# Kernel tuning notes

Hardware: AMD Instinct MI355X
Metric: run time of the kernel (lower is better)

Reference implementation:

```python
import jax, jax.numpy as jnp
import numpy as np

D_MODEL = 1024
D_INNER = 2048
D_STATE = 16
D_CONV = 4
DT_RANK = 64
BATCH = 2
SEQ = 1024


def _silu(v):
    return v * jax.nn.sigmoid(v)


def setup_inputs() -> dict:
    key = jax.random.key(0)
    ks = jax.random.split(key, 8)
    s = 0.02
    return {
        "x": jax.random.normal(ks[0], (BATCH, SEQ, D_MODEL), jnp.float32),
        "norm_w": jnp.ones((D_MODEL,), jnp.float32),
        "in_proj_w": (jax.random.normal(ks[1], (2 * D_INNER, D_MODEL), jnp.float32) * s),
        "conv_w": (jax.random.normal(ks[2], (D_INNER, 1, D_CONV), jnp.float32) * s),
        "conv_b": jnp.zeros((D_INNER,), jnp.float32),
        "x_proj_w": (jax.random.normal(ks[3], (DT_RANK + 2 * D_STATE, D_INNER), jnp.float32) * s),
        "dt_proj_w": (jax.random.normal(ks[4], (D_INNER, DT_RANK), jnp.float32) * s),
        "dt_proj_b": jnp.zeros((D_INNER,), jnp.float32),
        "A_log": jnp.log(jnp.broadcast_to(jnp.arange(1, D_STATE + 1, dtype=jnp.float32), (D_INNER, D_STATE))),
        "D": jnp.ones((D_INNER,), jnp.float32),
        "out_proj_w": (jax.random.normal(ks[5], (D_MODEL, D_INNER), jnp.float32) * s),
    }


def reference(x, norm_w, in_proj_w, conv_w, conv_b, x_proj_w, dt_proj_w, dt_proj_b, A_log, D, out_proj_w):
    b, l, d = x.shape
    x_copy = x
    # MambaRMSNorm
    h = x * jax.lax.rsqrt(jnp.mean(x * x, axis=-1, keepdims=True) + 1e-5) * norm_w
    # in_proj -> split into x-path and residual gate
    x_and_res = h @ in_proj_w.T                       # [b, l, 2*d_inner]
    xs, res = jnp.split(x_and_res, 2, axis=-1)
    # causal depthwise conv1d (torch pads d_conv-1 both sides then slices [:l])
    xc = jnp.transpose(xs, (0, 2, 1))                 # [b, d_inner, l]
    xc = jax.lax.conv_general_dilated(
        xc, conv_w, window_strides=(1,), padding=[(D_CONV - 1, 0)],
        feature_group_count=D_INNER, dimension_numbers=("NCH", "OIH", "NCH"))
    xc = xc + conv_b[None, :, None]
    u = _silu(jnp.transpose(xc, (0, 2, 1)))           # [b, l, d_inner]
    # SSM parameters
    A = -jnp.exp(A_log)                               # [d_inner, n]
    x_dbl = u @ x_proj_w.T                            # [b, l, dt_rank + 2n]
    delta, Bm, Cm = jnp.split(x_dbl, [DT_RANK, DT_RANK + D_STATE], axis=-1)
    delta = jax.nn.softplus(delta @ dt_proj_w.T + dt_proj_b)   # [b, l, d_inner]
    deltaA = jnp.exp(jnp.einsum("bld,dn->bldn", delta, A))     # [b, l, d_inner, n]
    deltaB_u = (delta * u)[..., None] * Bm[:, :, None, :]      # [b, l, d_inner, n]

    def step(state, inp):
        dA, dBu, c = inp                               # [b,d,n],[b,d,n],[b,n]
        state = dA * state + dBu
        y = jnp.einsum("bdn,bn->bd", state, c)
        return state, y

    init = jnp.zeros((b, D_INNER, D_STATE), dtype=u.dtype)
    _, ys = jax.lax.scan(
        step, init,
        (jnp.transpose(deltaA, (1, 0, 2, 3)),
         jnp.transpose(deltaB_u, (1, 0, 2, 3)),
         jnp.transpose(Cm, (1, 0, 2))))
    y = jnp.transpose(ys, (1, 0, 2)) + u * D           # [b, l, d_inner]
    y = y * _silu(res)
    return y @ out_proj_w.T + x_copy
```

## Files before the change

kernel.cpp:

```cpp
#include <hip/hip_runtime.h>
#include <hip/hip_bf16.h>
#include <math.h>

constexpr int B_   = 2;
constexpr int L_   = 1024;
constexpr int DM   = 1024;
constexpr int DI   = 2048;
constexpr int NS   = 16;
constexpr int DTR  = 64;
constexpr int TOK  = B_ * L_;

typedef __attribute__((ext_vector_type(8))) short short8;
typedef __attribute__((ext_vector_type(4))) float f32x4;
using bf16 = __hip_bfloat16;

__device__ __forceinline__ float sigmoidf_(float v) {
    return 1.f / (1.f + __expf(-v));
}
__device__ __forceinline__ float softplusf_(float v) {
    return fmaxf(v, 0.f) + __logf(1.f + __expf(-fabsf(v)));
}

__device__ __forceinline__ f32x4 mfma16(short8 a, short8 b, f32x4 c) {
    return __builtin_amdgcn_mfma_f32_16x16x32_bf16(a, b, c, 0, 0, 0);
}

__global__ __launch_bounds__(256) void k_rmsnorm(
    const float* __restrict__ x, const float* __restrict__ w,
    bf16* __restrict__ hh, bf16* __restrict__ hl)
{
    int row = blockIdx.x;
    const float4* xrp = (const float4*)(x + (size_t)row * DM);
    float4 v = xrp[threadIdx.x];
    float ss = v.x*v.x + v.y*v.y + v.z*v.z + v.w*v.w;
    #pragma unroll
    for (int m = 32; m >= 1; m >>= 1) ss += __shfl_xor(ss, m);
    __shared__ float acc[4];
    int wid = threadIdx.x >> 6, lane = threadIdx.x & 63;
    if (lane == 0) acc[wid] = ss;
    __syncthreads();
    float tot = acc[0] + acc[1] + acc[2] + acc[3];
    float sc = rsqrtf(tot * (1.f / DM) + 1e-5f);
    float4 wv = ((const float4*)w)[threadIdx.x];
    float o[4] = { v.x*sc*wv.x, v.y*sc*wv.y, v.z*sc*wv.z, v.w*sc*wv.w };
    alignas(8) bf16 H[4], Lo[4];
    #pragma unroll
    for (int j = 0; j < 4; ++j) {
        H[j]  = __float2bfloat16(o[j]);
        Lo[j] = __float2bfloat16(o[j] - __bfloat162float(H[j]));
    }
    size_t base = (size_t)row * DM + threadIdx.x * 4;
    *(ushort4*)(hh + base) = *(ushort4*)H;
    *(ushort4*)(hl + base) = *(ushort4*)Lo;
}

__global__ __launch_bounds__(256) void k_split(
    const float* __restrict__ s, bf16* __restrict__ hi, bf16* __restrict__ lo, int n4)
{
    int i = blockIdx.x * 256 + threadIdx.x;
    if (i >= n4) return;
    float4 v = ((const float4*)s)[i];
    float f[4] = { v.x, v.y, v.z, v.w };
    alignas(8) bf16 H[4], Lo[4];
    #pragma unroll
    for (int j = 0; j < 4; ++j) {
        H[j]  = __float2bfloat16(f[j]);
        Lo[j] = __float2bfloat16(f[j] - __bfloat162float(H[j]));
    }
    *(ushort4*)(hi + (size_t)i * 4) = *(ushort4*)H;
    *(ushort4*)(lo + (size_t)i * 4) = *(ushort4*)Lo;
}

__device__ __forceinline__ void stage_tile(const bf16* src, int ld, bf16* lds, int lane)
{
    #pragma unroll
    for (int j = 0; j < 8; ++j) {
        int c = (j << 6) + lane;
        int r = c >> 2;
        int g = (c & 3) ^ ((r >> 1) & 3);
        __builtin_amdgcn_global_load_lds(
            (const __attribute__((address_space(1))) unsigned int*)(src + (size_t)r * ld + (g << 3)),
            (__attribute__((address_space(3))) unsigned int*)(lds + (j << 9)),
            16, 0, 0);
    }
}

template<int NA, int EPI>
__global__ __launch_bounds__(256) void k_gemm_bf16(
    const bf16* __restrict__ Ah, const bf16* __restrict__ Al,
    const bf16* __restrict__ Bh, const bf16* __restrict__ Bl,
    float* __restrict__ C, const float* __restrict__ resid,
    int M, int N, int K)
{
    __shared__ alignas(1024) bf16 sA[2][NA][128 * 32];
    __shared__ alignas(1024) bf16 sB[2][2][128 * 32];

    int tid = threadIdx.x, lane = tid & 63, wv = tid >> 6;
    int bm0 = blockIdx.y * 128, bn0 = blockIdx.x * 128;
    int nkt = K >> 5;

    auto stage_all = [&](int buf, int kt) {
        int k0 = kt << 5;
        if constexpr (NA == 2) {
            if      (wv == 0) stage_tile(Ah + (size_t)bm0 * K + k0, K, &sA[buf][0][0], lane);
            else if (wv == 1) stage_tile(Al + (size_t)bm0 * K + k0, K, &sA[buf][1][0], lane);
            else if (wv == 2) stage_tile(Bh + (size_t)bn0 * K + k0, K, &sB[buf][0][0], lane);
            else              stage_tile(Bl + (size_t)bn0 * K + k0, K, &sB[buf][1][0], lane);
        } else {
            if      (wv == 0) stage_tile(Ah + (size_t)bm0 * K + k0, K, &sA[buf][0][0], lane);
            else if (wv == 1) stage_tile(Bh + (size_t)bn0 * K + k0, K, &sB[buf][0][0], lane);
            else if (wv == 2) stage_tile(Bl + (size_t)bn0 * K + k0, K, &sB[buf][1][0], lane);
        }
    };
    auto frag = [&](const bf16* t, int r, int g) -> short8 {
        int c = (r << 2) + (g ^ ((r >> 1) & 3));
        return *(const short8*)(t + (c << 3));
    };

    int wr = (wv >> 1) << 6;
    int wc = (wv & 1) << 6;
    int fr = lane & 15, g = lane >> 4;

    f32x4 acc[4][4] = {};

    stage_all(0, 0);
    __syncthreads();
    for (int kt = 0; kt < nkt; ++kt) {
        int cur = kt & 1;
        if (kt + 1 < nkt) stage_all(cur ^ 1, kt + 1);
        short8 a0[4], a1[4], b0[4], b1[4];
        #pragma unroll
        for (int m = 0; m < 4; ++m) {
            a0[m] = frag(&sA[cur][0][0], wr + m * 16 + fr, g);
            if constexpr (NA == 2) a1[m] = frag(&sA[cur][NA - 1][0], wr + m * 16 + fr, g);
        }
        #pragma unroll
        for (int n = 0; n < 4; ++n) {
            b0[n] = frag(&sB[cur][0][0], wc + n * 16 + fr, g);
            b1[n] = frag(&sB[cur][1][0], wc + n * 16 + fr, g);
        }
        #pragma unroll
        for (int m = 0; m < 4; ++m)
            #pragma unroll
            for (int n = 0; n < 4; ++n) {
                acc[m][n] = mfma16(a0[m], b0[n], acc[m][n]);
                acc[m][n] = mfma16(a0[m], b1[n], acc[m][n]);
                if constexpr (NA == 2) acc[m][n] = mfma16(a1[m], b0[n], acc[m][n]);
            }
        __syncthreads();
    }

    int rbase = bm0 + wr + (g << 2);
    int cb = bn0 + wc + fr;
    #pragma unroll
    for (int m = 0; m < 4; ++m)
        #pragma unroll
        for (int i = 0; i < 4; ++i) {
            int row = rbase + m * 16 + i;
            #pragma unroll
            for (int n = 0; n < 4; ++n) {
                int col = cb + n * 16;
                float v = acc[m][n][i];
                if constexpr (EPI == 2) v += resid[(size_t)row * N + col];
                C[(size_t)row * N + col] = v;
            }
        }
}

template<int EPI>
__global__ __launch_bounds__(256) void k_gemm_nt(
    const float* __restrict__ A, int lda,
    const float* __restrict__ Bm, int ldb,
    float* __restrict__ C, int ldc,
    int M, int N, int K_chunk,
    const float* __restrict__ bias)
{
    __shared__ float As[16][68];
    __shared__ float Bs[16][68];

    int tid = threadIdx.x;
    int m0 = blockIdx.y * 64;
    int n0 = blockIdx.x * 64;
    int kbase = blockIdx.z * K_chunk;

    int lr = tid >> 2;
    int lq = tid & 3;
    int ty = tid >> 4;
    int tx = tid & 15;

    float acc[4][4] = {};

    const float* Aptr = A + (size_t)(m0 + lr) * lda + kbase + lq * 4;
    int bn = n0 + lr;
    bool bvalid = bn < N;
    const float* Bptr = Bm + (size_t)(bvalid ? bn : 0) * ldb + kbase + lq * 4;

    for (int k0 = 0; k0 < K_chunk; k0 += 16) {
        float4 av = *(const float4*)(Aptr + k0);
        float4 bv = bvalid ? *(const float4*)(Bptr + k0)
                           : make_float4(0.f, 0.f, 0.f, 0.f);
        __syncthreads();
        As[lq*4+0][lr] = av.x; As[lq*4+1][lr] = av.y;
        As[lq*4+2][lr] = av.z; As[lq*4+3][lr] = av.w;
        Bs[lq*4+0][lr] = bv.x; Bs[lq*4+1][lr] = bv.y;
        Bs[lq*4+2][lr] = bv.z; Bs[lq*4+3][lr] = bv.w;
        __syncthreads();
        #pragma unroll
        for (int kk = 0; kk < 16; kk++) {
            float av_[4], bv_[4];
            *(float4*)av_ = *(const float4*)&As[kk][ty * 4];
            *(float4*)bv_ = *(const float4*)&Bs[kk][tx * 4];
            #pragma unroll
            for (int i = 0; i < 4; i++)
                #pragma unroll
                for (int j = 0; j < 4; j++)
                    acc[i][j] = fmaf(av_[i], bv_[j], acc[i][j]);
        }
    }

    int col = n0 + tx * 4;
    #pragma unroll
    for (int i = 0; i < 4; i++) {
        int row = m0 + ty * 4 + i;
        if constexpr (EPI == 3) {
            #pragma unroll
            for (int j = 0; j < 4; j++)
                if (col + j < N)
                    atomicAdd(&C[(size_t)row * ldc + col + j], acc[i][j]);
        } else {
            float vv[4];
            #pragma unroll
            for (int j = 0; j < 4; j++)
                vv[j] = softplusf_(acc[i][j] + bias[col + j]);
            *(float4*)&C[(size_t)row * ldc + col] = *(float4*)vv;
        }
    }
}

__global__ __launch_bounds__(256) void k_conv_silu(
    const float* __restrict__ xr, const float* __restrict__ w,
    const float* __restrict__ bconv, float* __restrict__ u)
{
    int idx = blockIdx.x * 256 + threadIdx.x;
    int dq = idx & 511;
    int l  = (idx >> 9) & 1023;
    int bb = idx >> 19;
    int dd = dq * 4;

    float4 wrow[4];
    #pragma unroll
    for (int j = 0; j < 4; j++)
        wrow[j] = *(const float4*)&w[(dd + j) * 4];
    float4 bias4 = *(const float4*)&bconv[dd];

    float acc[4] = { bias4.x, bias4.y, bias4.z, bias4.w };
    #pragma unroll
    for (int k = 0; k < 4; k++) {
        int lp = l - 3 + k;
        if (lp >= 0) {
            const float4 xv = *(const float4*)
                &xr[((size_t)(bb * L_ + lp)) * (2 * DI) + dd];
            const float xs_[4] = { xv.x, xv.y, xv.z, xv.w };
            #pragma unroll
            for (int j = 0; j < 4; j++)
                acc[j] = fmaf(xs_[j], ((const float*)&wrow[j])[k], acc[j]);
        }
    }
    float out[4];
    #pragma unroll
    for (int j = 0; j < 4; j++)
        out[j] = acc[j] * sigmoidf_(acc[j]);
    *(float4*)&u[((size_t)(bb * L_ + l)) * DI + dd] = *(float4*)out;
}

__global__ __launch_bounds__(256) void k_scan_part(
    const float* __restrict__ delta, const float* __restrict__ u,
    const float* __restrict__ xdbl, const float* __restrict__ A_log,
    float* __restrict__ P, float* __restrict__ S)
{
    int bx = blockIdx.x;
    int c  = bx & 7;
    int rest = bx >> 3;
    int b  = rest >> 7;
    int d0 = (rest & 127) << 4;
    int t = threadIdx.x;
    int cl = t >> 4, n = t & 15;
    int d = d0 + cl;

    float A_dn = -__expf(A_log[d * NS + n]);
    float p = 1.f, s = 0.f;
    size_t tokbase = (size_t)b * L_ + (c << 7);
    #pragma unroll 4
    for (int k = 0; k < 128; ++k) {
        size_t tok = tokbase + k;
        float dl = delta[tok * DI + d];
        float uu = u[tok * DI + d];
        float Bv = xdbl[tok * 96 + 64 + n];
        float dA = __expf(dl * A_dn);
        s = fmaf(dA, s, dl * uu * Bv);
        p *= dA;
    }
    size_t o = ((((size_t)b * 8 + c) * DI) + d) * NS + n;
    P[o] = p; S[o] = s;
}

__global__ __launch_bounds__(256) void k_scan_comb(
    const float* __restrict__ P, const float* __restrict__ S,
    float* __restrict__ init)
{
    int idx = blockIdx.x * 256 + threadIdx.x;
    int n = idx & 15;
    int d = (idx >> 4) & (DI - 1);
    int b = idx >> 15;
    float carry = 0.f;
    #pragma unroll
    for (int c = 0; c < 8; ++c) {
        size_t o = ((((size_t)b * 8 + c) * DI) + d) * NS + n;
        init[o] = carry;
        carry = fmaf(P[o], carry, S[o]);
    }
}

__global__ __launch_bounds__(256) void k_scan_y(
    const float* __restrict__ delta, const float* __restrict__ u,
    const float* __restrict__ xdbl, const float* __restrict__ xr,
    const float* __restrict__ A_log, const float* __restrict__ Dp,
    const float* __restrict__ init, bf16* __restrict__ y)
{
    int bx = blockIdx.x;
    int c  = bx & 7;
    int rest = bx >> 3;
    int b  = rest >> 7;
    int d0 = (rest & 127) << 4;
    int t = threadIdx.x;
    int cl = t >> 4, n = t & 15;
    int d = d0 + cl;

    float A_dn = -__expf(A_log[d * NS + n]);
    float Dd = Dp[d];
    size_t o = ((((size_t)b * 8 + c) * DI) + d) * NS + n;
    float s = init[o];
    size_t tokbase = (size_t)b * L_ + (c << 7);
    #pragma unroll 4
    for (int k = 0; k < 128; ++k) {
        size_t tok = tokbase + k;
        float dl = delta[tok * DI + d];
        float uu = u[tok * DI + d];
        float Bv = xdbl[tok * 96 + 64 + n];
        float Cv = xdbl[tok * 96 + 80 + n];
        float dA = __expf(dl * A_dn);
        s = fmaf(dA, s, dl * uu * Bv);
        float py = s * Cv;
        py += __shfl_xor(py, 1);
        py += __shfl_xor(py, 2);
        py += __shfl_xor(py, 4);
        py += __shfl_xor(py, 8);
        if (n == 0) {
            float r = xr[tok * (2 * DI) + DI + d];
            float yv = fmaf(uu, Dd, py) * (r * sigmoidf_(r));
            y[tok * DI + d] = __float2bfloat16(yv);
        }
    }
}

extern "C" void kernel_launch(void* const* d_in, const int* in_sizes, int n_in,
                              void* d_out, int out_size, void* d_ws, size_t ws_size,
                              hipStream_t stream)
{
    const float* x       = (const float*)d_in[0];
    const float* norm_w  = (const float*)d_in[1];
    const float* in_proj = (const float*)d_in[2];
    const float* conv_w  = (const float*)d_in[3];
    const float* conv_b  = (const float*)d_in[4];
    const float* x_proj  = (const float*)d_in[5];
    const float* dt_w    = (const float*)d_in[6];
    const float* dt_b    = (const float*)d_in[7];
    const float* A_log   = (const float*)d_in[8];
    const float* Dp      = (const float*)d_in[9];
    const float* out_w   = (const float*)d_in[10];
    float* out = (float*)d_out;

    constexpr size_t MB = 1u << 20;
    char* Wb = (char*)d_ws;
    float* xr    = (float*)(Wb + 0);
    bf16*  h_h   = (bf16*) (Wb + 32 * MB);
    bf16*  h_l   = (bf16*) (Wb + 36 * MB);
    float* u     = (float*)(Wb + 32 * MB);
    float* delta = (float*)(Wb + 48 * MB);
    bf16*  wo_h  = (bf16*) (Wb + 48 * MB);
    bf16*  wo_l  = (bf16*) (Wb + 52 * MB);
    bf16*  wi_h  = (bf16*) (Wb + 64 * MB);
    bf16*  wi_l  = (bf16*) (Wb + 72 * MB);
    float* Pbuf  = (float*)(Wb + 64 * MB);
    float* Sbuf  = (float*)(Wb + 66 * MB);
    bf16*  y_h   = (bf16*) (Wb + 68 * MB);
    float* initb = (float*)(Wb + 76 * MB);
    float* xdbl  = (float*)(Wb + 78 * MB);

    k_rmsnorm<<<TOK, 256, 0, stream>>>(x, norm_w, h_h, h_l);
    k_split<<<4096, 256, 0, stream>>>(in_proj, wi_h, wi_l, (2 * DI * DM) / 4);
    k_gemm_bf16<2, 0><<<dim3(32, 16), 256, 0, stream>>>(
        h_h, h_l, wi_h, wi_l, xr, nullptr, TOK, 2 * DI, DM);
    k_conv_silu<<<4096, 256, 0, stream>>>(xr, conv_w, conv_b, u);
    hipMemsetAsync(xdbl, 0, (size_t)TOK * 96 * sizeof(float), stream);
    k_gemm_nt<3><<<dim3(2, 32, 8), 256, 0, stream>>>(
        u, DI, x_proj, DI, xdbl, 96, TOK, 96, DI / 8, nullptr);
    k_gemm_nt<1><<<dim3(32, 32, 1), 256, 0, stream>>>(
        xdbl, 96, dt_w, DTR, delta, DI, TOK, DI, DTR, dt_b);
    k_scan_part<<<2048, 256, 0, stream>>>(delta, u, xdbl, A_log, Pbuf, Sbuf);
    k_scan_comb<<<256, 256, 0, stream>>>(Pbuf, Sbuf, initb);
    k_scan_y<<<2048, 256, 0, stream>>>(delta, u, xdbl, xr, A_log, Dp, initb, y_h);
    k_split<<<2048, 256, 0, stream>>>(out_w, wo_h, wo_l, (DM * DI) / 4);
    k_gemm_bf16<1, 2><<<dim3(8, 16), 256, 0, stream>>>(
        y_h, nullptr, wo_h, wo_l, out, x, TOK, DM, DI);
}
```

Baseline: 413.0 us.

## Move x_proj and dt_proj GEMMs to split-bf16 MFMA and batch scan output reduction

Replaces the fp32 SIMT GEMM kernel used for x_proj and dt_proj with the existing split-bf16 MFMA GEMM, now generalised with leading dimensions, split-K atomics and a softplus-bias epilogue. The conv kernel emits hi/lo bf16 copies of u, and extra split kernels convert x_proj (zero-padded to 128 rows), dt_w and xdbl. The scan output kernel processes 16-token segments and does a transposed butterfly reduction, so each lane writes one token's output instead of every step needing a 4-shuffle reduce with a single writer. This adds conversion passes, extra workspace traffic and padded GEMM work, and reshuffles buffer aliasing, including reusing Sbuf in place as the scan init.

```diff
diff --git a/kernel.cpp b/kernel.cpp
--- a/kernel.cpp
+++ b/kernel.cpp
@@ -71,6 +71,26 @@
     *(ushort4*)(lo + (size_t)i * 4) = *(ushort4*)Lo;
 }
 
+__global__ __launch_bounds__(256) void k_split_pad(
+    const float* __restrict__ s, bf16* __restrict__ hi, bf16* __restrict__ lo)
+{
+    int i = blockIdx.x * 256 + threadIdx.x;
+    int row = i >> 9;
+    float f[4] = {0.f, 0.f, 0.f, 0.f};
+    if (row < 96) {
+        float4 v = ((const float4*)s)[i];
+        f[0] = v.x; f[1] = v.y; f[2] = v.z; f[3] = v.w;
+    }
+    alignas(8) bf16 H[4], Lo[4];
+    #pragma unroll
+    for (int j = 0; j < 4; ++j) {
+        H[j]  = __float2bfloat16(f[j]);
+        Lo[j] = __float2bfloat16(f[j] - __bfloat162float(H[j]));
+    }
+    *(ushort4*)(hi + (size_t)i * 4) = *(ushort4*)H;
+    *(ushort4*)(lo + (size_t)i * 4) = *(ushort4*)Lo;
+}
+
 __device__ __forceinline__ void stage_tile(const bf16* src, int ld, bf16* lds, int lane)
 {
     #pragma unroll
@@ -87,29 +107,36 @@
 
 template<int NA, int EPI>
 __global__ __launch_bounds__(256) void k_gemm_bf16(
-    const bf16* __restrict__ Ah, const bf16* __restrict__ Al,
-    const bf16* __restrict__ Bh, const bf16* __restrict__ Bl,
-    float* __restrict__ C, const float* __restrict__ resid,
-    int M, int N, int K)
+    const bf16* __restrict__ Ah, const bf16* __restrict__ Al, int lda,
+    const bf16* __restrict__ Bh, const bf16* __restrict__ Bl, int ldb,
+    float* __restrict__ C, int ldc,
+    const float* __restrict__ aux,
+    int M, int Nb, int Kc)
 {
     __shared__ alignas(1024) bf16 sA[2][NA][128 * 32];
     __shared__ alignas(1024) bf16 sB[2][2][128 * 32];
 
     int tid = threadIdx.x, lane = tid & 63, wv = tid >> 6;
     int bm0 = blockIdx.y * 128, bn0 = blockIdx.x * 128;
-    int nkt = K >> 5;
+    int kbase = blockIdx.z * Kc;
+    int nkt = Kc >> 5;
+
+    const bf16* Abase_h = Ah + (size_t)bm0 * lda + kbase;
+    const bf16* Abase_l = (NA == 2) ? (Al + (size_t)bm0 * lda + kbase) : nullptr;
+    const bf16* Bbase_h = Bh + (size_t)bn0 * ldb + kbase;
+    const bf16* Bbase_l = Bl + (size_t)bn0 * ldb + kbase;
 
     auto stage_all = [&](int buf, int kt) {
         int k0 = kt << 5;
         if constexpr (NA == 2) {
-            if      (wv == 0) stage_tile(Ah + (size_t)bm0 * K + k0, K, &sA[buf][0][0], lane);
-            else if (wv == 1) stage_tile(Al + (size_t)bm0 * K + k0, K, &sA[buf][1][0], lane);
-            else if (wv == 2) stage_tile(Bh + (size_t)bn0 * K + k0, K, &sB[buf][0][0], lane);
-            else              stage_tile(Bl + (size_t)bn0 * K + k0, K, &sB[buf][1][0], lane);
+            if      (wv == 0) stage_tile(Abase_h + k0, lda, &sA[buf][0][0], lane);
+            else if (wv == 1) stage_tile(Abase_l + k0, lda, &sA[buf][1][0], lane);
+            else if (wv == 2) stage_tile(Bbase_h + k0, ldb, &sB[buf][0][0], lane);
+            else              stage_tile(Bbase_l + k0, ldb, &sB[buf][1][0], lane);
         } else {
-            if      (wv == 0) stage_tile(Ah + (size_t)bm0 * K + k0, K, &sA[buf][0][0], lane);
-            else if (wv == 1) stage_tile(Bh + (size_t)bn0 * K + k0, K, &sB[buf][0][0], lane);
-            else if (wv == 2) stage_tile(Bl + (size_t)bn0 * K + k0, K, &sB[buf][1][0], lane);
+            if      (wv == 0) stage_tile(Abase_h + k0, lda, &sA[buf][0][0], lane);
+            else if (wv == 1) stage_tile(Bbase_h + k0, ldb, &sB[buf][0][0], lane);
+            else if (wv == 2) stage_tile(Bbase_l + k0, ldb, &sB[buf][1][0], lane);
         }
     };
     auto frag = [&](const bf16* t, int r, int g) -> short8 {
@@ -161,85 +188,21 @@
             for (int n = 0; n < 4; ++n) {
                 int col = cb + n * 16;
                 float v = acc[m][n][i];
-                if constexpr (EPI == 2) v += resid[(size_t)row * N + col];
-                C[(size_t)row * N + col] = v;
+                if constexpr (EPI == 3) {
+                    if (col < Nb) atomicAdd(&C[(size_t)row * ldc + col], v);
+                } else {
+                    if constexpr (EPI == 1) v = softplusf_(v + aux[col]);
+                    if constexpr (EPI == 2) v += aux[(size_t)row * ldc + col];
+                    C[(size_t)row * ldc + col] = v;
+                }
             }
         }
-}
-
-template<int EPI>
-__global__ __launch_bounds__(256) void k_gemm_nt(
-    const float* __restrict__ A, int lda,
-    const float* __restrict__ Bm, int ldb,
-    float* __restrict__ C, int ldc,
-    int M, int N, int K_chunk,
-    const float* __restrict__ bias)
-{
-    __shared__ float As[16][68];
-    __shared__ float Bs[16][68];
-
-    int tid = threadIdx.x;
-    int m0 = blockIdx.y * 64;
-    int n0 = blockIdx.x * 64;
-    int kbase = blockIdx.z * K_chunk;
-
-    int lr = tid >> 2;
-    int lq = tid & 3;
-    int ty = tid >> 4;
-    int tx = tid & 15;
-
-    float acc[4][4] = {};
-
-    const float* Aptr = A + (size_t)(m0 + lr) * lda + kbase + lq * 4;
-    int bn = n0 + lr;
-    bool bvalid = bn < N;
-    const float* Bptr = Bm + (size_t)(bvalid ? bn : 0) * ldb + kbase + lq * 4;
-
-    for (int k0 = 0; k0 < K_chunk; k0 += 16) {
-        float4 av = *(const float4*)(Aptr + k0);
-        float4 bv = bvalid ? *(const float4*)(Bptr + k0)
-                           : make_float4(0.f, 0.f, 0.f, 0.f);
-        __syncthreads();
-        As[lq*4+0][lr] = av.x; As[lq*4+1][lr] = av.y;
-        As[lq*4+2][lr] = av.z; As[lq*4+3][lr] = av.w;
-        Bs[lq*4+0][lr] = bv.x; Bs[lq*4+1][lr] = bv.y;
-        Bs[lq*4+2][lr] = bv.z; Bs[lq*4+3][lr] = bv.w;
-        __syncthreads();
-        #pragma unroll
-        for (int kk = 0; kk < 16; kk++) {
-            float av_[4], bv_[4];
-            *(float4*)av_ = *(const float4*)&As[kk][ty * 4];
-            *(float4*)bv_ = *(const float4*)&Bs[kk][tx * 4];
-            #pragma unroll
-            for (int i = 0; i < 4; i++)
-                #pragma unroll
-                for (int j = 0; j < 4; j++)
-                    acc[i][j] = fmaf(av_[i], bv_[j], acc[i][j]);
-        }
-    }
-
-    int col = n0 + tx * 4;
-    #pragma unroll
-    for (int i = 0; i < 4; i++) {
-        int row = m0 + ty * 4 + i;
-        if constexpr (EPI == 3) {
-            #pragma unroll
-            for (int j = 0; j < 4; j++)
-                if (col + j < N)
-                    atomicAdd(&C[(size_t)row * ldc + col + j], acc[i][j]);
-        } else {
-            float vv[4];
-            #pragma unroll
-            for (int j = 0; j < 4; j++)
-                vv[j] = softplusf_(acc[i][j] + bias[col + j]);
-            *(float4*)&C[(size_t)row * ldc + col] = *(float4*)vv;
-        }
-    }
 }
 
 __global__ __launch_bounds__(256) void k_conv_silu(
     const float* __restrict__ xr, const float* __restrict__ w,
-    const float* __restrict__ bconv, float* __restrict__ u)
+    const float* __restrict__ bconv, float* __restrict__ u,
+    bf16* __restrict__ uh, bf16* __restrict__ ul)
 {
     int idx = blockIdx.x * 256 + threadIdx.x;
     int dq = idx & 511;
@@ -267,10 +230,17 @@
         }
     }
     float out[4];
-    #pragma unroll
-    for (int j = 0; j < 4; j++)
+    alignas(8) bf16 H[4], Lo[4];
+    #pragma unroll
+    for (int j = 0; j < 4; j++) {
         out[j] = acc[j] * sigmoidf_(acc[j]);
-    *(float4*)&u[((size_t)(bb * L_ + l)) * DI + dd] = *(float4*)out;
+        H[j]  = __float2bfloat16(out[j]);
+        Lo[j] = __float2bfloat16(out[j] - __bfloat162float(H[j]));
+    }
+    size_t base = ((size_t)(bb * L_ + l)) * DI + dd;
+    *(float4*)&u[base] = *(float4*)out;
+    *(ushort4*)(uh + base) = *(ushort4*)H;
+    *(ushort4*)(ul + base) = *(ushort4*)Lo;
 }
 
 __global__ __launch_bounds__(256) void k_scan_part(
@@ -305,8 +275,7 @@
 }
 
 __global__ __launch_bounds__(256) void k_scan_comb(
-    const float* __restrict__ P, const float* __restrict__ S,
-    float* __restrict__ init)
+    const float* __restrict__ P, float* __restrict__ S)
 {
     int idx = blockIdx.x * 256 + threadIdx.x;
     int n = idx & 15;
@@ -316,8 +285,9 @@
     #pragma unroll
     for (int c = 0; c < 8; ++c) {
         size_t o = ((((size_t)b * 8 + c) * DI) + d) * NS + n;
-        init[o] = carry;
-        carry = fmaf(P[o], carry, S[o]);
+        float Pv = P[o], Sv = S[o];
+        S[o] = carry;
+        carry = fmaf(Pv, carry, Sv);
     }
 }
 
@@ -341,25 +311,40 @@
     size_t o = ((((size_t)b * 8 + c) * DI) + d) * NS + n;
     float s = init[o];
     size_t tokbase = (size_t)b * L_ + (c << 7);
-    #pragma unroll 4
-    for (int k = 0; k < 128; ++k) {
-        size_t tok = tokbase + k;
-        float dl = delta[tok * DI + d];
-        float uu = u[tok * DI + d];
-        float Bv = xdbl[tok * 96 + 64 + n];
-        float Cv = xdbl[tok * 96 + 80 + n];
-        float dA = __expf(dl * A_dn);
-        s = fmaf(dA, s, dl * uu * Bv);
-        float py = s * Cv;
-        py += __shfl_xor(py, 1);
-        py += __shfl_xor(py, 2);
-        py += __shfl_xor(py, 4);
-        py += __shfl_xor(py, 8);
-        if (n == 0) {
-            float r = xr[tok * (2 * DI) + DI + d];
-            float yv = fmaf(uu, Dd, py) * (r * sigmoidf_(r));
-            y[tok * DI + d] = __float2bfloat16(yv);
-        }
+
+    for (int seg = 0; seg < 8; ++seg) {
+        size_t segbase = tokbase + seg * 16;
+        float v[16];
+        float uu_mine = 0.f;
+        #pragma unroll
+        for (int k = 0; k < 16; ++k) {
+            size_t tok = segbase + k;
+            float dl = delta[tok * DI + d];
+            float uu = u[tok * DI + d];
+            float Bv = xdbl[tok * 96 + 64 + n];
+            float Cv = xdbl[tok * 96 + 80 + n];
+            float dA = __expf(dl * A_dn);
+            s = fmaf(dA, s, dl * uu * Bv);
+            v[k] = s * Cv;
+            uu_mine = (k == n) ? uu : uu_mine;
+        }
+        #pragma unroll
+        for (int m = 8; m >= 1; m >>= 1) {
+            bool up = (n & m) != 0;
+            #pragma unroll
+            for (int i = 0; i < 8; ++i) {
+                if (i < m) {
+                    float sent = up ? v[i] : v[i + m];
+                    float got = __shfl_xor(sent, m);
+                    float kept = up ? v[i + m] : v[i];
+                    v[i] = kept + got;
+                }
+            }
+        }
+        size_t tokm = segbase + n;
+        float rr = xr[tokm * (2 * DI) + DI + d];
+        float yv = fmaf(uu_mine, Dd, v[0]) * (rr * sigmoidf_(rr));
+        y[tokm * DI + d] = __float2bfloat16(yv);
     }
 }
 
@@ -381,36 +366,47 @@
     float* out = (float*)d_out;
 
     constexpr size_t MB = 1u << 20;
+    constexpr size_t KB = 1u << 10;
     char* Wb = (char*)d_ws;
-    float* xr    = (float*)(Wb + 0);
-    bf16*  h_h   = (bf16*) (Wb + 32 * MB);
-    bf16*  h_l   = (bf16*) (Wb + 36 * MB);
-    float* u     = (float*)(Wb + 32 * MB);
-    float* delta = (float*)(Wb + 48 * MB);
-    bf16*  wo_h  = (bf16*) (Wb + 48 * MB);
-    bf16*  wo_l  = (bf16*) (Wb + 52 * MB);
-    bf16*  wi_h  = (bf16*) (Wb + 64 * MB);
-    bf16*  wi_l  = (bf16*) (Wb + 72 * MB);
-    float* Pbuf  = (float*)(Wb + 64 * MB);
-    float* Sbuf  = (float*)(Wb + 66 * MB);
-    bf16*  y_h   = (bf16*) (Wb + 68 * MB);
-    float* initb = (float*)(Wb + 76 * MB);
-    float* xdbl  = (float*)(Wb + 78 * MB);
+    float* xr     = (float*)(Wb + 0);
+    bf16*  h_h    = (bf16*) (Wb + 32 * MB);
+    bf16*  h_l    = (bf16*) (Wb + 36 * MB);
+    float* u      = (float*)(Wb + 32 * MB);
+    bf16*  u_h    = (bf16*) (Wb + 48 * MB);
+    bf16*  u_l    = (bf16*) (Wb + 56 * MB);
+    float* delta  = (float*)(Wb + 48 * MB);
+    bf16*  wi_h   = (bf16*) (Wb + 64 * MB);
+    bf16*  wi_l   = (bf16*) (Wb + 72 * MB);
+    bf16*  wo_h   = (bf16*) (Wb + 64 * MB);
+    bf16*  wo_l   = (bf16*) (Wb + 68 * MB);
+    bf16*  xp_h   = (bf16*) (Wb + 72 * MB);
+    bf16*  xp_l   = (bf16*) (Wb + 73 * MB);
+    float* Pbuf   = (float*)(Wb + 72 * MB);
+    bf16*  y_h    = (bf16*) (Wb + 72 * MB);
+    float* xdbl   = (float*)(Wb + 80 * MB);
+    bf16*  xdbl_h = (bf16*) (Wb + 81 * MB);
+    bf16*  xdbl_l = (bf16*) (Wb + 81 * MB + 512 * KB);
+    bf16*  dtw_h  = (bf16*) (Wb + 82 * MB);
+    bf16*  dtw_l  = (bf16*) (Wb + 82 * MB + 256 * KB);
+    float* Sbuf   = (float*)(Wb + 82 * MB + 512 * KB);
 
     k_rmsnorm<<<TOK, 256, 0, stream>>>(x, norm_w, h_h, h_l);
     k_split<<<4096, 256, 0, stream>>>(in_proj, wi_h, wi_l, (2 * DI * DM) / 4);
-    k_gemm_bf16<2, 0><<<dim3(32, 16), 256, 0, stream>>>(
-        h_h, h_l, wi_h, wi_l, xr, nullptr, TOK, 2 * DI, DM);
-    k_conv_silu<<<4096, 256, 0, stream>>>(xr, conv_w, conv_b, u);
+    k_gemm_bf16<2, 0><<<dim3(32, 16, 1), 256, 0, stream>>>(
+        h_h, h_l, DM, wi_h, wi_l, DM, xr, 2 * DI, nullptr, TOK, 2 * DI, DM);
+    k_split<<<2048, 256, 0, stream>>>(out_w, wo_h, wo_l, (DM * DI) / 4);
+    k_conv_silu<<<4096, 256, 0, stream>>>(xr, conv_w, conv_b, u, u_h, u_l);
+    k_split_pad<<<256, 256, 0, stream>>>(x_proj, xp_h, xp_l);
     hipMemsetAsync(xdbl, 0, (size_t)TOK * 96 * sizeof(float), stream);
-    k_gemm_nt<3><<<dim3(2, 32, 8), 256, 0, stream>>>(
-        u, DI, x_proj, DI, xdbl, 96, TOK, 96, DI / 8, nullptr);
-    k_gemm_nt<1><<<dim3(32, 32, 1), 256, 0, stream>>>(
-        xdbl, 96, dt_w, DTR, delta, DI, TOK, DI, DTR, dt_b);
+    k_gemm_bf16<2, 3><<<dim3(1, 16, 8), 256, 0, stream>>>(
+        u_h, u_l, DI, xp_h, xp_l, DI, xdbl, 96, nullptr, TOK, 96, DI / 8);
+    k_split<<<128, 256, 0, stream>>>(dt_w, dtw_h, dtw_l, (DI * DTR) / 4);
+    k_split<<<192, 256, 0, stream>>>(xdbl, xdbl_h, xdbl_l, (TOK * 96) / 4);
+    k_gemm_bf16<2, 1><<<dim3(16, 16, 1), 256, 0, stream>>>(
+        xdbl_h, xdbl_l, 96, dtw_h, dtw_l, DTR, delta, DI, dt_b, TOK, DI, DTR);
     k_scan_part<<<2048, 256, 0, stream>>>(delta, u, xdbl, A_log, Pbuf, Sbuf);
-    k_scan_comb<<<256, 256, 0, stream>>>(Pbuf, Sbuf, initb);
-    k_scan_y<<<2048, 256, 0, stream>>>(delta, u, xdbl, xr, A_log, Dp, initb, y_h);
-    k_split<<<2048, 256, 0, stream>>>(out_w, wo_h, wo_l, (DM * DI) / 4);
-    k_gemm_bf16<1, 2><<<dim3(8, 16), 256, 0, stream>>>(
-        y_h, nullptr, wo_h, wo_l, out, x, TOK, DM, DI);
-}
+    k_scan_comb<<<256, 256, 0, stream>>>(Pbuf, Sbuf);
+    k_scan_y<<<2048, 256, 0, stream>>>(delta, u, xdbl, xr, A_log, Dp, Sbuf, y_h);
+    k_gemm_bf16<1, 2><<<dim3(8, 16, 1), 256, 0, stream>>>(
+        y_h, nullptr, DI, wo_h, wo_l, DI, out, DM, x, TOK, DM, DI);
+}
```

New measurement: 438.4 us. 1.06x slower.
